# Performance work log

Measured on AMD Instinct MI355X. Metric: run time of the kernel, lower is better.

The kernel has to match this reference:

```python
import jax, jax.numpy as jnp
import numpy as np

N = 100000
E = 1600000
D = 128      # in_features
H = 128      # mlp hidden = out_features
O = 128      # out_features
BN_EPS = 1e-5

def _bn_train(x, gamma, beta):
    # BatchNorm1d in training mode: batch stats over node axis, biased variance
    mu = jnp.mean(x, axis=0)
    var = jnp.mean((x - mu) ** 2, axis=0)
    return (x - mu) * jax.lax.rsqrt(var + BN_EPS) * gamma + beta

def setup_inputs() -> dict:
    key = jax.random.key(0)
    ks = jax.random.split(key, 8)
    h = jax.random.normal(ks[0], (N, D), dtype=jnp.float32)
    edge_src = jax.random.randint(ks[1], (E,), 0, N, dtype=jnp.int32)
    edge_dst = jax.random.randint(ks[2], (E,), 0, N, dtype=jnp.int32)
    s1 = 1.0 / np.sqrt(D)
    s2 = 1.0 / np.sqrt(H)
    W1 = jax.random.uniform(ks[3], (D, H), jnp.float32, -s1, s1)
    b1 = jax.random.uniform(ks[4], (H,), jnp.float32, -s1, s1)
    W2 = jax.random.uniform(ks[5], (H, O), jnp.float32, -s2, s2)
    b2 = jax.random.uniform(ks[6], (O,), jnp.float32, -s2, s2)
    return {
        "h": h, "edge_src": edge_src, "edge_dst": edge_dst,
        "W1": W1, "b1": b1, "g1": jnp.ones((H,), jnp.float32), "be1": jnp.zeros((H,), jnp.float32),
        "W2": W2, "b2": b2, "g2": jnp.ones((O,), jnp.float32), "be2": jnp.zeros((O,), jnp.float32),
        "eps": jnp.zeros((), jnp.float32),
    }

def reference(h, edge_src, edge_dst, W1, b1, g1, be1, W2, b2, g2, be2, eps):
    # spmm(Adj, h) == scatter-add of gathered neighbor features
    msgs = h[edge_src]                                   # [E, D] irregular gather
    pooled = jax.ops.segment_sum(msgs, edge_dst, num_segments=N)  # [N, D]
    pooled = pooled + (1.0 + eps) * h                    # eps combine
    # MLP (2 layers): Linear -> BN -> ReLU -> Linear
    x = jax.nn.relu(_bn_train(pooled @ W1 + b1, g1, be1))
    x = x @ W2 + b2
    # final BN + ReLU
    return jax.nn.relu(_bn_train(x, g2, be2))
```

## Files before the change

kernel.cpp:

```cpp
#include <hip/hip_runtime.h>
#include <hip/hip_bf16.h>
#include <stdint.h>

#define BN_EPS 1e-5f
#define NSTRIPE 64

typedef __attribute__((ext_vector_type(8)))  short bf16x8;
typedef __attribute__((ext_vector_type(16))) float f32x16;

static __device__ __forceinline__ float bflo2f(uint32_t p){
  union { uint32_t u; float f; } c; c.u = p << 16; return c.f;
}
static __device__ __forceinline__ float bfhi2f(uint32_t p){
  union { uint32_t u; float f; } c; c.u = p & 0xffff0000u; return c.f;
}
static __device__ __forceinline__ uint16_t f2bf(float f){
  union { float f; uint32_t u; } c; c.f = f;
  uint32_t u = c.u;
  return (uint16_t)((u + 0x7fffu + ((u >> 16) & 1u)) >> 16);
}
static __device__ __forceinline__ uint32_t pack2(float a, float b){
  return (uint32_t)f2bf(a) | ((uint32_t)f2bf(b) << 16);
}

__global__ void k_prep(const float* __restrict__ h, uint16_t* __restrict__ hb, int hblocks,
                       const float* __restrict__ W1, const float* __restrict__ W2,
                       uint16_t* __restrict__ Wt1, uint16_t* __restrict__ Wt2,
                       float* __restrict__ stats,
                       const int* __restrict__ dst, int* __restrict__ M, int E, int NB){
  int b = blockIdx.x, t = threadIdx.x;
  if (b < hblocks){
    int i = (b * 256 + t) * 8;
    float4 a = *(const float4*)(h + i);
    float4 bb = *(const float4*)(h + i + 4);
    uint4 o;
    o.x = pack2(a.x, a.y); o.y = pack2(a.z, a.w);
    o.z = pack2(bb.x, bb.y); o.w = pack2(bb.z, bb.w);
    *(uint4*)(hb + i) = o;
    return;
  }
  if (b < hblocks + 16){
    int gid = (b - hblocks) * 256 + t;
    {
      float4 z = make_float4(0.f, 0.f, 0.f, 0.f);
      *(float4*)(stats + gid * 8) = z;
      *(float4*)(stats + gid * 8 + 4) = z;
    }
    const float* Wf = (gid < 2048) ? W1 : W2;
    uint16_t* Wt = (gid < 2048) ? Wt1 : Wt2;
    int cid = gid & 2047;
    int nrow = cid >> 4;
    int c    = cid & 15;
    int k0 = c * 8;
    float e[8];
    #pragma unroll
    for (int j = 0; j < 8; ++j) e[j] = Wf[(k0 + j) * 128 + nrow];
    uint4 o;
    o.x = pack2(e[0], e[1]); o.y = pack2(e[2], e[3]);
    o.z = pack2(e[4], e[5]); o.w = pack2(e[6], e[7]);
    int cs = c ^ (nrow & 15);
    *(uint4*)(Wt + nrow * 128 + cs * 8) = o;
    return;
  }
  int eb = b - hblocks - 16;
  __shared__ int cnt[512];
  cnt[t] = 0; cnt[t + 256] = 0;
  __syncthreads();
  int base = eb * 4096;
  #pragma unroll 4
  for (int j = t; j < 4096; j += 256){
    int i = base + j;
    if (i < E) atomicAdd(&cnt[dst[i] >> 8], 1);
  }
  __syncthreads();
  size_t row = (size_t)eb * NB;
  if (t < NB) M[row + t] = cnt[t];
  int t2 = t + 256;
  if (t2 < NB) M[row + t2] = cnt[t2];
}

__global__ void k_colscan(int* __restrict__ M, int* __restrict__ btot, int EB, int NB){
  __shared__ int s[256];
  int b = blockIdx.x, t = threadIdx.x;
  int i0 = 2 * t, i1 = 2 * t + 1;
  int v0 = (i0 < EB) ? M[(size_t)i0 * NB + b] : 0;
  int v1 = (i1 < EB) ? M[(size_t)i1 * NB + b] : 0;
  s[t] = v0 + v1;
  __syncthreads();
  for (int off = 1; off < 256; off <<= 1){
    int v = (t >= off) ? s[t - off] : 0;
    __syncthreads();
    s[t] += v;
    __syncthreads();
  }
  int excl = s[t] - (v0 + v1);
  if (i0 < EB) M[(size_t)i0 * NB + b] = excl;
  if (i1 < EB) M[(size_t)i1 * NB + b] = excl + v0;
  if (t == 255) btot[b] = s[255];
}

__global__ void k_bscan(const int* __restrict__ btot, int* __restrict__ bbase,
                        int* __restrict__ row_off, int NB, int n, int E){
  __shared__ int s[256];
  int t = threadIdx.x;
  int i0 = 2 * t, i1 = 2 * t + 1;
  int v0 = (i0 < NB) ? btot[i0] : 0;
  int v1 = (i1 < NB) ? btot[i1] : 0;
  s[t] = v0 + v1;
  __syncthreads();
  for (int off = 1; off < 256; off <<= 1){
    int v = (t >= off) ? s[t - off] : 0;
    __syncthreads();
    s[t] += v;
    __syncthreads();
  }
  int excl = s[t] - (v0 + v1);
  if (i0 < NB) bbase[i0] = excl;
  if (i1 < NB) bbase[i1] = excl + v0;
  if (t == 0){ bbase[NB] = E; row_off[n] = E; }
}

__global__ void k_bin(const int* __restrict__ src, const int* __restrict__ dst,
                      const int* __restrict__ M, const int* __restrict__ bbase,
                      uint2* __restrict__ binned, int E, int NB){
  __shared__ int comb[512];
  __shared__ int cur[512];
  int t = threadIdx.x;
  size_t row = (size_t)blockIdx.x * NB;
  if (t < NB) comb[t] = bbase[t] + M[row + t];
  int t2 = t + 256;
  if (t2 < NB) comb[t2] = bbase[t2] + M[row + t2];
  cur[t] = 0; cur[t + 256] = 0;
  __syncthreads();
  int base = blockIdx.x * 4096;
  #pragma unroll 4
  for (int j = t; j < 4096; j += 256){
    int i = base + j;
    if (i < E){
      int d = dst[i];
      int b = d >> 8;
      int r = atomicAdd(&cur[b], 1);
      binned[comb[b] + r] = make_uint2((unsigned)src[i], (unsigned)d);
    }
  }
}

__global__ void k_csr(const uint2* __restrict__ binned, const int* __restrict__ bbase,
                      int* __restrict__ row_off, int* __restrict__ col_idx, int n){
  __shared__ int cnt[256];
  __shared__ int off[256];
  __shared__ int cur[256];
  int b = blockIdx.x, t = threadIdx.x;
  int e0 = bbase[b], e1 = bbase[b + 1];
  int nb0 = b << 8;
  cnt[t] = 0; cur[t] = 0;
  __syncthreads();
  int m = e1 - e0;
  for (int j = t; j < m; j += 256) atomicAdd(&cnt[binned[e0 + j].y & 255], 1);
  __syncthreads();
  int v = cnt[t];
  off[t] = v;
  __syncthreads();
  for (int o = 1; o < 256; o <<= 1){
    int u = (t >= o) ? off[t - o] : 0;
    __syncthreads();
    off[t] += u;
    __syncthreads();
  }
  int excl = off[t] - v;
  __syncthreads();
  off[t] = excl;
  if (nb0 + t < n) row_off[nb0 + t] = e0 + excl;
  __syncthreads();
  for (int j = t; j < m; j += 256){
    uint2 p = binned[e0 + j];
    int dl = p.y & 255;
    int r = atomicAdd(&cur[dl], 1);
    col_idx[e0 + off[dl] + r] = (int)p.x;
  }
}

__global__ void k_gather(const uint16_t* __restrict__ hb, const int* __restrict__ row_off,
                         const int* __restrict__ col_idx, const float* __restrict__ eps_p,
                         uint16_t* __restrict__ Xb, int n){
  int node = (blockIdx.x << 2) + (threadIdx.x >> 6);
  int lane = threadIdx.x & 63;
  if (node >= n) return;
  int g = lane >> 4;
  int c = lane & 15;
  const uint4* hp4 = (const uint4*)hb;
  int j = row_off[node], jend = row_off[node + 1];
  float a0=0.f,a1=0.f,a2=0.f,a3=0.f,a4=0.f,a5=0.f,a6=0.f,a7=0.f;
  for (; j + 16 <= jend; j += 16){
    int sA = col_idx[j + g];
    int sB = col_idx[j + 4 + g];
    int sC = col_idx[j + 8 + g];
    int sD = col_idx[j + 12 + g];
    uint4 vA = hp4[(size_t)sA * 16 + c];
    uint4 vB = hp4[(size_t)sB * 16 + c];
    uint4 vC = hp4[(size_t)sC * 16 + c];
    uint4 vD = hp4[(size_t)sD * 16 + c];
    a0 += (bflo2f(vA.x) + bflo2f(vB.x)) + (bflo2f(vC.x) + bflo2f(vD.x));
    a1 += (bfhi2f(vA.x) + bfhi2f(vB.x)) + (bfhi2f(vC.x) + bfhi2f(vD.x));
    a2 += (bflo2f(vA.y) + bflo2f(vB.y)) + (bflo2f(vC.y) + bflo2f(vD.y));
    a3 += (bfhi2f(vA.y) + bfhi2f(vB.y)) + (bfhi2f(vC.y) + bfhi2f(vD.y));
    a4 += (bflo2f(vA.z) + bflo2f(vB.z)) + (bflo2f(vC.z) + bflo2f(vD.z));
    a5 += (bfhi2f(vA.z) + bfhi2f(vB.z)) + (bfhi2f(vC.z) + bfhi2f(vD.z));
    a6 += (bflo2f(vA.w) + bflo2f(vB.w)) + (bflo2f(vC.w) + bflo2f(vD.w));
    a7 += (bfhi2f(vA.w) + bfhi2f(vB.w)) + (bfhi2f(vC.w) + bfhi2f(vD.w));
  }
  for (; j + 8 <= jend; j += 8){
    int sA = col_idx[j + g];
    int sB = col_idx[j + 4 + g];
    uint4 vA = hp4[(size_t)sA * 16 + c];
    uint4 vB = hp4[(size_t)sB * 16 + c];
    a0 += bflo2f(vA.x) + bflo2f(vB.x);
    a1 += bfhi2f(vA.x) + bfhi2f(vB.x);
    a2 += bflo2f(vA.y) + bflo2f(vB.y);
    a3 += bfhi2f(vA.y) + bfhi2f(vB.y);
    a4 += bflo2f(vA.z) + bflo2f(vB.z);
    a5 += bfhi2f(vA.z) + bfhi2f(vB.z);
    a6 += bflo2f(vA.w) + bflo2f(vB.w);
    a7 += bfhi2f(vA.w) + bfhi2f(vB.w);
  }
  for (; j + 4 <= jend; j += 4){
    int s = col_idx[j + g];
    uint4 v = hp4[(size_t)s * 16 + c];
    a0 += bflo2f(v.x); a1 += bfhi2f(v.x);
    a2 += bflo2f(v.y); a3 += bfhi2f(v.y);
    a4 += bflo2f(v.z); a5 += bfhi2f(v.z);
    a6 += bflo2f(v.w); a7 += bfhi2f(v.w);
  }
  int rem = jend - j;
  if (rem > 0){
    int jj = j + (g < rem ? g : rem - 1);
    float w = (g < rem) ? 1.f : 0.f;
    int s = col_idx[jj];
    uint4 v = hp4[(size_t)s * 16 + c];
    a0 = fmaf(w, bflo2f(v.x), a0); a1 = fmaf(w, bfhi2f(v.x), a1);
    a2 = fmaf(w, bflo2f(v.y), a2); a3 = fmaf(w, bfhi2f(v.y), a3);
    a4 = fmaf(w, bflo2f(v.z), a4); a5 = fmaf(w, bfhi2f(v.z), a5);
    a6 = fmaf(w, bflo2f(v.w), a6); a7 = fmaf(w, bfhi2f(v.w), a7);
  }
  a0 += __shfl_xor(a0, 16); a1 += __shfl_xor(a1, 16);
  a2 += __shfl_xor(a2, 16); a3 += __shfl_xor(a3, 16);
  a4 += __shfl_xor(a4, 16); a5 += __shfl_xor(a5, 16);
  a6 += __shfl_xor(a6, 16); a7 += __shfl_xor(a7, 16);
  a0 += __shfl_xor(a0, 32); a1 += __shfl_xor(a1, 32);
  a2 += __shfl_xor(a2, 32); a3 += __shfl_xor(a3, 32);
  a4 += __shfl_xor(a4, 32); a5 += __shfl_xor(a5, 32);
  a6 += __shfl_xor(a6, 32); a7 += __shfl_xor(a7, 32);
  if (g == 0){
    float ce = 1.0f + eps_p[0];
    uint4 vh = hp4[(size_t)node * 16 + c];
    a0 = fmaf(ce, bflo2f(vh.x), a0); a1 = fmaf(ce, bfhi2f(vh.x), a1);
    a2 = fmaf(ce, bflo2f(vh.y), a2); a3 = fmaf(ce, bfhi2f(vh.y), a3);
    a4 = fmaf(ce, bflo2f(vh.z), a4); a5 = fmaf(ce, bfhi2f(vh.z), a5);
    a6 = fmaf(ce, bflo2f(vh.w), a6); a7 = fmaf(ce, bfhi2f(vh.w), a7);
    uint4 o;
    o.x = pack2(a0, a1); o.y = pack2(a2, a3);
    o.z = pack2(a4, a5); o.w = pack2(a6, a7);
    *((uint4*)Xb + (size_t)node * 16 + c) = o;
  }
}

template<bool BN_IN>
__global__ __launch_bounds__(256, 3) void k_mgemm(
    const uint16_t* __restrict__ Ag, const uint16_t* __restrict__ Wt,
    const float* __restrict__ bias_f,
    const float* __restrict__ sin_s, const float* __restrict__ sqin_s,
    const float* __restrict__ gin, const float* __restrict__ bein, float invN,
    uint16_t* __restrict__ Yout, float* __restrict__ osum_s, float* __restrict__ osq_s, int n){
  __shared__ __align__(16) uint16_t Al[64 * 128];
  __shared__ __align__(16) uint16_t Wl[128 * 128];
  __shared__ float csum[128], csq[128];
  __shared__ __align__(16) float ABl[256];
  int tid = threadIdx.x;
  int rbase = blockIdx.x * 64;
  int stripe = blockIdx.x & (NSTRIPE - 1);

  if (BN_IN){
    if (tid < 128){
      float s = 0.f, q = 0.f;
      #pragma unroll 8
      for (int st = 0; st < NSTRIPE; ++st){
        s += sin_s[st * 128 + tid];
        q += sqin_s[st * 128 + tid];
      }
      float mu = s * invN;
      float var = q * invN - mu * mu;
      float A = gin[tid] * rsqrtf(var + BN_EPS);
      ABl[tid] = A;
      ABl[128 + tid] = bein[tid] - mu * A;
    }
    __syncthreads();
  }

  {
    const uint4* g = (const uint4*)Wt;
    uint4* d = (uint4*)Wl;
    #pragma unroll
    for (int i = 0; i < 8; ++i) d[tid + 256 * i] = g[tid + 256 * i];
  }
  #pragma unroll
  for (int i = 0; i < 4; ++i){
    int f = tid + 256 * i;
    int m = f >> 4, c = f & 15;
    int gr = rbase + m;
    uint4 v = make_uint4(0, 0, 0, 0);
    if (gr < n){
      v = *(const uint4*)(Ag + (size_t)gr * 128 + c * 8);
      if (BN_IN){
        int k0 = c * 8;
        float4 ka0 = *(const float4*)(ABl + k0);
        float4 ka1 = *(const float4*)(ABl + k0 + 4);
        float4 kb0 = *(const float4*)(ABl + 128 + k0);
        float4 kb1 = *(const float4*)(ABl + 128 + k0 + 4);
        float e0 = fmaxf(fmaf(bflo2f(v.x), ka0.x, kb0.x), 0.f);
        float e1 = fmaxf(fmaf(bfhi2f(v.x), ka0.y, kb0.y), 0.f);
        float e2 = fmaxf(fmaf(bflo2f(v.y), ka0.z, kb0.z), 0.f);
        float e3 = fmaxf(fmaf(bfhi2f(v.y), ka0.w, kb0.w), 0.f);
        float e4 = fmaxf(fmaf(bflo2f(v.z), ka1.x, kb1.x), 0.f);
        float e5 = fmaxf(fmaf(bfhi2f(v.z), ka1.y, kb1.y), 0.f);
        float e6 = fmaxf(fmaf(bflo2f(v.w), ka1.z, kb1.z), 0.f);
        float e7 = fmaxf(fmaf(bfhi2f(v.w), ka1.w, kb1.w), 0.f);
        v.x = pack2(e0, e1); v.y = pack2(e2, e3);
        v.z = pack2(e4, e5); v.w = pack2(e6, e7);
      }
    }
    *(uint4*)((char*)Al + m * 256 + ((c ^ (m & 15)) * 16)) = v;
  }
  if (tid < 128){ csum[tid] = 0.f; csq[tid] = 0.f; }
  __syncthreads();

  int lane = tid & 63;
  int w    = tid >> 6;
  int hi   = lane >> 5;
  int key  = lane & 15;
  int m0   = (w & 1) * 32;
  int n0   = (w >> 1) * 64;
  int mrow = m0 + (lane & 31);
  int nrow0 = n0 + (lane & 31);
  int nrow1 = nrow0 + 32;

  f32x16 acc0, acc1;
  #pragma unroll
  for (int i = 0; i < 16; ++i){ acc0[i] = 0.f; acc1[i] = 0.f; }

  const char* Ab = (const char*)Al;
  const char* Wb = (const char*)Wl;
  #pragma unroll
  for (int kt = 0; kt < 8; ++kt){
    int cs = ((2 * kt + hi) ^ key) * 16;
    bf16x8 a  = *(const bf16x8*)(Ab + mrow  * 256 + cs);
    bf16x8 b0 = *(const bf16x8*)(Wb + nrow0 * 256 + cs);
    bf16x8 b1 = *(const bf16x8*)(Wb + nrow1 * 256 + cs);
    acc0 = __builtin_amdgcn_mfma_f32_32x32x16_bf16(a, b0, acc0, 0, 0, 0);
    acc1 = __builtin_amdgcn_mfma_f32_32x32x16_bf16(a, b1, acc1, 0, 0, 0);
  }
  __syncthreads();

  uint16_t* Yl = Wl;
  float bias0 = bias_f[nrow0];
  float bias1 = bias_f[nrow1];
  float ps0 = 0.f, pq0 = 0.f, ps1 = 0.f, pq1 = 0.f;
  #pragma unroll
  for (int r = 0; r < 16; ++r){
    int row = m0 + (r & 3) + 8 * (r >> 2) + 4 * hi;
    bool valid = (rbase + row) < n;
    float y0 = acc0[r] + bias0;
    float y1 = acc1[r] + bias1;
    if (valid){
      ps0 += y0; pq0 += y0 * y0;
      ps1 += y1; pq1 += y1 * y1;
    }
    Yl[row * 128 + nrow0] = f2bf(y0);
    Yl[row * 128 + nrow1] = f2bf(y1);
  }
  atomicAdd(&csum[nrow0], ps0); atomicAdd(&csq[nrow0], pq0);
  atomicAdd(&csum[nrow1], ps1); atomicAdd(&csq[nrow1], pq1);
  __syncthreads();

  #pragma unroll
  for (int i = 0; i < 4; ++i){
    int id = tid + 256 * i;
    int row = id >> 4, c = id & 15;
    int gr = rbase + row;
    if (gr < n)
      *((uint4*)Yout + (size_t)gr * 16 + c) = *((const uint4*)Yl + id);
  }
  if (tid < 128){
    atomicAdd(&osum_s[stripe * 128 + tid], csum[tid]);
    atomicAdd(&osq_s[stripe * 128 + tid], csq[tid]);
  }
}

__global__ void k_bncoef2(const float* __restrict__ sum_s, const float* __restrict__ sq_s,
                          const float* __restrict__ g, const float* __restrict__ be,
                          float* __restrict__ AB, float invN){
  int c = threadIdx.x;
  if (c < 128){
    float s = 0.f, q = 0.f;
    #pragma unroll 8
    for (int st = 0; st < NSTRIPE; ++st){
      s += sum_s[st * 128 + c];
      q += sq_s[st * 128 + c];
    }
    float mu = s * invN;
    float var = q * invN - mu * mu;
    float A = g[c] * rsqrtf(var + BN_EPS);
    AB[c] = A;
    AB[128 + c] = be[c] - mu * A;
  }
}

__global__ void k_final(const uint16_t* __restrict__ Y2b, const float* __restrict__ ABg,
                        float* __restrict__ out, int total){
  __shared__ __align__(16) float AB[256];
  int tid = threadIdx.x;
  if (tid < 64){
    *(float4*)(AB + tid * 4) = *(const float4*)(ABg + tid * 4);
  }
  __syncthreads();
  int i = (blockIdx.x * 256 + tid) * 4;
  if (i >= total) return;
  uint2 v = *(const uint2*)(Y2b + i);
  int c = i & 127;
  float4 a = *(const float4*)(AB + c);
  float4 b = *(const float4*)(AB + 128 + c);
  float4 o;
  o.x = fmaxf(fmaf(bflo2f(v.x), a.x, b.x), 0.f);
  o.y = fmaxf(fmaf(bfhi2f(v.x), a.y, b.y), 0.f);
  o.z = fmaxf(fmaf(bflo2f(v.y), a.z, b.z), 0.f);
  o.w = fmaxf(fmaf(bfhi2f(v.y), a.w, b.w), 0.f);
  *(float4*)(out + i) = o;
}

extern "C" void kernel_launch(void* const* d_in, const int* in_sizes, int n_in,
                              void* d_out, int out_size, void* d_ws, size_t ws_size,
                              hipStream_t stream){
  const float* h    = (const float*)d_in[0];
  const int*   esrc = (const int*)d_in[1];
  const int*   edst = (const int*)d_in[2];
  const float* W1   = (const float*)d_in[3];
  const float* b1   = (const float*)d_in[4];
  const float* g1   = (const float*)d_in[5];
  const float* be1  = (const float*)d_in[6];
  const float* W2   = (const float*)d_in[7];
  const float* b2   = (const float*)d_in[8];
  const float* g2   = (const float*)d_in[9];
  const float* be2  = (const float*)d_in[10];
  const float* eps  = (const float*)d_in[11];
  int n = in_sizes[0] / 128;
  int E = in_sizes[1];
  (void)n_in; (void)out_size; (void)ws_size;

  int NB = (n + 255) >> 8;
  int EB = (E + 4095) >> 12;

  char* ws = (char*)d_ws;
  size_t off = 0;
  auto alloc = [&](size_t bytes) -> void* {
    void* p = ws + off;
    off += (bytes + 511) & ~(size_t)511;
    return p;
  };
  size_t feat_b = (size_t)n * 128 * 2;
  uint16_t* B1   = (uint16_t*)alloc(feat_b);
  uint16_t* B2   = (uint16_t*)alloc(feat_b);
  int*   row_off = (int*)alloc((size_t)(n + 1) * 4);
  int*   col_idx = (int*)alloc((size_t)E * 4);
  int*   M       = (int*)alloc((size_t)EB * NB * 4);
  int*   btot    = (int*)alloc((size_t)(NB + 1) * 4);
  int*   bbase   = (int*)alloc((size_t)(NB + 1) * 4);
  float* stats   = (float*)alloc((size_t)4 * NSTRIPE * 128 * 4);
  float* AB2     = (float*)alloc(256 * 4);
  uint16_t* Wt1  = (uint16_t*)alloc(128 * 128 * 2);
  uint16_t* Wt2  = (uint16_t*)alloc(128 * 128 * 2);
  float* sum1 = stats;
  float* sq1  = stats + NSTRIPE * 128;
  float* sum2 = stats + 2 * NSTRIPE * 128;
  float* sq2  = stats + 3 * NSTRIPE * 128;
  uint16_t* hb  = B1;
  uint2*   binned = (uint2*)B2;
  uint16_t* Xb  = B2;
  uint16_t* Y1b = B1;
  uint16_t* Y2b = B2;

  int total = n * 128;
  int hblocks = total / 8 / 256;
  float invN = 1.0f / (float)n;

  k_prep<<<hblocks + 16 + EB, 256, 0, stream>>>(h, hb, hblocks, W1, W2, Wt1, Wt2,
                                                stats, edst, M, E, NB);
  k_colscan<<<NB, 256, 0, stream>>>(M, btot, EB, NB);
  k_bscan  <<<1, 256, 0, stream>>>(btot, bbase, row_off, NB, n, E);
  k_bin    <<<EB, 256, 0, stream>>>(esrc, edst, M, bbase, binned, E, NB);
  k_csr    <<<NB, 256, 0, stream>>>(binned, bbase, row_off, col_idx, n);

  k_gather<<<(n + 3) / 4, 256, 0, stream>>>(hb, row_off, col_idx, eps, Xb, n);

  int gblocks = (n + 63) / 64;
  k_mgemm<false><<<gblocks, 256, 0, stream>>>(Xb, Wt1, b1,
      nullptr, nullptr, nullptr, nullptr, 0.f, Y1b, sum1, sq1, n);
  k_mgemm<true> <<<gblocks, 256, 0, stream>>>(Y1b, Wt2, b2,
      sum1, sq1, g1, be1, invN, Y2b, sum2, sq2, n);

  k_bncoef2<<<1, 128, 0, stream>>>(sum2, sq2, g2, be2, AB2, invN);
  k_final<<<(total / 4 + 255) / 256, 256, 0, stream>>>(Y2b, AB2, (float*)d_out, total);
}
```

Baseline: 309.9 us.

## Fuse neighbor gather into first GEMM and read weights from global

Merges the gather/aggregation kernel with the first MFMA GEMM: each block aggregates 64 node rows directly into shared memory and multiplies by W1. This removes the intermediate pooled-feature write and read and one kernel launch. Both GEMM kernels also stop staging the transposed weights in LDS and read B fragments straight from global (unswizzled layout), which cuts LDS use to allow higher occupancy. The trade-off is less parallelism in the gather phase (each wave handles 16 nodes serially) and B operands now come through L1/L2 instead of LDS.

```diff
diff --git a/kernel.cpp b/kernel.cpp
--- a/kernel.cpp
+++ b/kernel.cpp
@@ -58,8 +58,7 @@
     uint4 o;
     o.x = pack2(e[0], e[1]); o.y = pack2(e[2], e[3]);
     o.z = pack2(e[4], e[5]); o.w = pack2(e[6], e[7]);
-    int cs = c ^ (nrow & 15);
-    *(uint4*)(Wt + nrow * 128 + cs * 8) = o;
+    *(uint4*)(Wt + nrow * 128 + c * 8) = o;
     return;
   }
   int eb = b - hblocks - 16;
@@ -180,128 +179,180 @@
   }
 }
 
-__global__ void k_gather(const uint16_t* __restrict__ hb, const int* __restrict__ row_off,
-                         const int* __restrict__ col_idx, const float* __restrict__ eps_p,
-                         uint16_t* __restrict__ Xb, int n){
-  int node = (blockIdx.x << 2) + (threadIdx.x >> 6);
-  int lane = threadIdx.x & 63;
-  if (node >= n) return;
+__global__ __launch_bounds__(256, 4) void k_gg(
+    const uint16_t* __restrict__ hb, const int* __restrict__ row_off,
+    const int* __restrict__ col_idx, const float* __restrict__ eps_p,
+    const uint16_t* __restrict__ Wt, const float* __restrict__ bias_f,
+    uint16_t* __restrict__ Yout, float* __restrict__ osum_s, float* __restrict__ osq_s, int n){
+  __shared__ __align__(16) uint16_t Al[64 * 128];
+  __shared__ float csum[128], csq[128];
+  int tid = threadIdx.x;
+  int rbase = blockIdx.x * 64;
+  int stripe = blockIdx.x & (NSTRIPE - 1);
+  int lane = tid & 63;
+  int w    = tid >> 6;
   int g = lane >> 4;
   int c = lane & 15;
   const uint4* hp4 = (const uint4*)hb;
-  int j = row_off[node], jend = row_off[node + 1];
-  float a0=0.f,a1=0.f,a2=0.f,a3=0.f,a4=0.f,a5=0.f,a6=0.f,a7=0.f;
-  for (; j + 16 <= jend; j += 16){
-    int sA = col_idx[j + g];
-    int sB = col_idx[j + 4 + g];
-    int sC = col_idx[j + 8 + g];
-    int sD = col_idx[j + 12 + g];
-    uint4 vA = hp4[(size_t)sA * 16 + c];
-    uint4 vB = hp4[(size_t)sB * 16 + c];
-    uint4 vC = hp4[(size_t)sC * 16 + c];
-    uint4 vD = hp4[(size_t)sD * 16 + c];
-    a0 += (bflo2f(vA.x) + bflo2f(vB.x)) + (bflo2f(vC.x) + bflo2f(vD.x));
-    a1 += (bfhi2f(vA.x) + bfhi2f(vB.x)) + (bfhi2f(vC.x) + bfhi2f(vD.x));
-    a2 += (bflo2f(vA.y) + bflo2f(vB.y)) + (bflo2f(vC.y) + bflo2f(vD.y));
-    a3 += (bfhi2f(vA.y) + bfhi2f(vB.y)) + (bfhi2f(vC.y) + bfhi2f(vD.y));
-    a4 += (bflo2f(vA.z) + bflo2f(vB.z)) + (bflo2f(vC.z) + bflo2f(vD.z));
-    a5 += (bfhi2f(vA.z) + bfhi2f(vB.z)) + (bfhi2f(vC.z) + bfhi2f(vD.z));
-    a6 += (bflo2f(vA.w) + bflo2f(vB.w)) + (bflo2f(vC.w) + bflo2f(vD.w));
-    a7 += (bfhi2f(vA.w) + bfhi2f(vB.w)) + (bfhi2f(vC.w) + bfhi2f(vD.w));
-  }
-  for (; j + 8 <= jend; j += 8){
-    int sA = col_idx[j + g];
-    int sB = col_idx[j + 4 + g];
-    uint4 vA = hp4[(size_t)sA * 16 + c];
-    uint4 vB = hp4[(size_t)sB * 16 + c];
-    a0 += bflo2f(vA.x) + bflo2f(vB.x);
-    a1 += bfhi2f(vA.x) + bfhi2f(vB.x);
-    a2 += bflo2f(vA.y) + bflo2f(vB.y);
-    a3 += bfhi2f(vA.y) + bfhi2f(vB.y);
-    a4 += bflo2f(vA.z) + bflo2f(vB.z);
-    a5 += bfhi2f(vA.z) + bfhi2f(vB.z);
-    a6 += bflo2f(vA.w) + bflo2f(vB.w);
-    a7 += bfhi2f(vA.w) + bfhi2f(vB.w);
-  }
-  for (; j + 4 <= jend; j += 4){
-    int s = col_idx[j + g];
-    uint4 v = hp4[(size_t)s * 16 + c];
-    a0 += bflo2f(v.x); a1 += bfhi2f(v.x);
-    a2 += bflo2f(v.y); a3 += bfhi2f(v.y);
-    a4 += bflo2f(v.z); a5 += bfhi2f(v.z);
-    a6 += bflo2f(v.w); a7 += bfhi2f(v.w);
-  }
-  int rem = jend - j;
-  if (rem > 0){
-    int jj = j + (g < rem ? g : rem - 1);
-    float w = (g < rem) ? 1.f : 0.f;
-    int s = col_idx[jj];
-    uint4 v = hp4[(size_t)s * 16 + c];
-    a0 = fmaf(w, bflo2f(v.x), a0); a1 = fmaf(w, bfhi2f(v.x), a1);
-    a2 = fmaf(w, bflo2f(v.y), a2); a3 = fmaf(w, bfhi2f(v.y), a3);
-    a4 = fmaf(w, bflo2f(v.z), a4); a5 = fmaf(w, bfhi2f(v.z), a5);
-    a6 = fmaf(w, bflo2f(v.w), a6); a7 = fmaf(w, bfhi2f(v.w), a7);
-  }
-  a0 += __shfl_xor(a0, 16); a1 += __shfl_xor(a1, 16);
-  a2 += __shfl_xor(a2, 16); a3 += __shfl_xor(a3, 16);
-  a4 += __shfl_xor(a4, 16); a5 += __shfl_xor(a5, 16);
-  a6 += __shfl_xor(a6, 16); a7 += __shfl_xor(a7, 16);
-  a0 += __shfl_xor(a0, 32); a1 += __shfl_xor(a1, 32);
-  a2 += __shfl_xor(a2, 32); a3 += __shfl_xor(a3, 32);
-  a4 += __shfl_xor(a4, 32); a5 += __shfl_xor(a5, 32);
-  a6 += __shfl_xor(a6, 32); a7 += __shfl_xor(a7, 32);
-  if (g == 0){
-    float ce = 1.0f + eps_p[0];
-    uint4 vh = hp4[(size_t)node * 16 + c];
-    a0 = fmaf(ce, bflo2f(vh.x), a0); a1 = fmaf(ce, bfhi2f(vh.x), a1);
-    a2 = fmaf(ce, bflo2f(vh.y), a2); a3 = fmaf(ce, bfhi2f(vh.y), a3);
-    a4 = fmaf(ce, bflo2f(vh.z), a4); a5 = fmaf(ce, bfhi2f(vh.z), a5);
-    a6 = fmaf(ce, bflo2f(vh.w), a6); a7 = fmaf(ce, bfhi2f(vh.w), a7);
-    uint4 o;
-    o.x = pack2(a0, a1); o.y = pack2(a2, a3);
-    o.z = pack2(a4, a5); o.w = pack2(a6, a7);
-    *((uint4*)Xb + (size_t)node * 16 + c) = o;
-  }
-}
-
-template<bool BN_IN>
-__global__ __launch_bounds__(256, 3) void k_mgemm(
+  float ce = 1.0f + eps_p[0];
+  if (tid < 128){ csum[tid] = 0.f; csq[tid] = 0.f; }
+
+  for (int it = 0; it < 16; ++it){
+    int m = w * 16 + it;
+    int gr = rbase + m;
+    float a0=0.f,a1=0.f,a2=0.f,a3=0.f,a4=0.f,a5=0.f,a6=0.f,a7=0.f;
+    if (gr < n){
+      int j = row_off[gr], jend = row_off[gr + 1];
+      for (; j + 16 <= jend; j += 16){
+        int sA = col_idx[j + g];
+        int sB = col_idx[j + 4 + g];
+        int sC = col_idx[j + 8 + g];
+        int sD = col_idx[j + 12 + g];
+        uint4 vA = hp4[(size_t)sA * 16 + c];
+        uint4 vB = hp4[(size_t)sB * 16 + c];
+        uint4 vC = hp4[(size_t)sC * 16 + c];
+        uint4 vD = hp4[(size_t)sD * 16 + c];
+        a0 += (bflo2f(vA.x) + bflo2f(vB.x)) + (bflo2f(vC.x) + bflo2f(vD.x));
+        a1 += (bfhi2f(vA.x) + bfhi2f(vB.x)) + (bfhi2f(vC.x) + bfhi2f(vD.x));
+        a2 += (bflo2f(vA.y) + bflo2f(vB.y)) + (bflo2f(vC.y) + bflo2f(vD.y));
+        a3 += (bfhi2f(vA.y) + bfhi2f(vB.y)) + (bfhi2f(vC.y) + bfhi2f(vD.y));
+        a4 += (bflo2f(vA.z) + bflo2f(vB.z)) + (bflo2f(vC.z) + bflo2f(vD.z));
+        a5 += (bfhi2f(vA.z) + bfhi2f(vB.z)) + (bfhi2f(vC.z) + bfhi2f(vD.z));
+        a6 += (bflo2f(vA.w) + bflo2f(vB.w)) + (bflo2f(vC.w) + bflo2f(vD.w));
+        a7 += (bfhi2f(vA.w) + bfhi2f(vB.w)) + (bfhi2f(vC.w) + bfhi2f(vD.w));
+      }
+      for (; j + 4 <= jend; j += 4){
+        int s = col_idx[j + g];
+        uint4 v = hp4[(size_t)s * 16 + c];
+        a0 += bflo2f(v.x); a1 += bfhi2f(v.x);
+        a2 += bflo2f(v.y); a3 += bfhi2f(v.y);
+        a4 += bflo2f(v.z); a5 += bfhi2f(v.z);
+        a6 += bflo2f(v.w); a7 += bfhi2f(v.w);
+      }
+      int rem = jend - j;
+      if (rem > 0){
+        int jj = j + (g < rem ? g : rem - 1);
+        float wq = (g < rem) ? 1.f : 0.f;
+        int s = col_idx[jj];
+        uint4 v = hp4[(size_t)s * 16 + c];
+        a0 = fmaf(wq, bflo2f(v.x), a0); a1 = fmaf(wq, bfhi2f(v.x), a1);
+        a2 = fmaf(wq, bflo2f(v.y), a2); a3 = fmaf(wq, bfhi2f(v.y), a3);
+        a4 = fmaf(wq, bflo2f(v.z), a4); a5 = fmaf(wq, bfhi2f(v.z), a5);
+        a6 = fmaf(wq, bflo2f(v.w), a6); a7 = fmaf(wq, bfhi2f(v.w), a7);
+      }
+      a0 += __shfl_xor(a0, 16); a1 += __shfl_xor(a1, 16);
+      a2 += __shfl_xor(a2, 16); a3 += __shfl_xor(a3, 16);
+      a4 += __shfl_xor(a4, 16); a5 += __shfl_xor(a5, 16);
+      a6 += __shfl_xor(a6, 16); a7 += __shfl_xor(a7, 16);
+      a0 += __shfl_xor(a0, 32); a1 += __shfl_xor(a1, 32);
+      a2 += __shfl_xor(a2, 32); a3 += __shfl_xor(a3, 32);
+      a4 += __shfl_xor(a4, 32); a5 += __shfl_xor(a5, 32);
+      a6 += __shfl_xor(a6, 32); a7 += __shfl_xor(a7, 32);
+      if (g == 0){
+        uint4 vh = hp4[(size_t)gr * 16 + c];
+        a0 = fmaf(ce, bflo2f(vh.x), a0); a1 = fmaf(ce, bfhi2f(vh.x), a1);
+        a2 = fmaf(ce, bflo2f(vh.y), a2); a3 = fmaf(ce, bfhi2f(vh.y), a3);
+        a4 = fmaf(ce, bflo2f(vh.z), a4); a5 = fmaf(ce, bfhi2f(vh.z), a5);
+        a6 = fmaf(ce, bflo2f(vh.w), a6); a7 = fmaf(ce, bfhi2f(vh.w), a7);
+      }
+    }
+    if (g == 0){
+      uint4 o;
+      o.x = pack2(a0, a1); o.y = pack2(a2, a3);
+      o.z = pack2(a4, a5); o.w = pack2(a6, a7);
+      *(uint4*)((char*)Al + m * 256 + ((c ^ (m & 15)) * 16)) = o;
+    }
+  }
+  __syncthreads();
+
+  int hi   = lane >> 5;
+  int key  = lane & 15;
+  int m0   = (w & 1) * 32;
+  int n0   = (w >> 1) * 64;
+  int mrow = m0 + (lane & 31);
+  int nrow0 = n0 + (lane & 31);
+  int nrow1 = nrow0 + 32;
+
+  f32x16 acc0, acc1;
+  #pragma unroll
+  for (int i = 0; i < 16; ++i){ acc0[i] = 0.f; acc1[i] = 0.f; }
+
+  const char* Ab = (const char*)Al;
+  #pragma unroll
+  for (int kt = 0; kt < 8; ++kt){
+    int ck = 2 * kt + hi;
+    bf16x8 a  = *(const bf16x8*)(Ab + mrow * 256 + ((ck ^ key) * 16));
+    bf16x8 b0 = *(const bf16x8*)(Wt + nrow0 * 128 + ck * 8);
+    bf16x8 b1 = *(const bf16x8*)(Wt + nrow1 * 128 + ck * 8);
+    acc0 = __builtin_amdgcn_mfma_f32_32x32x16_bf16(a, b0, acc0, 0, 0, 0);
+    acc1 = __builtin_amdgcn_mfma_f32_32x32x16_bf16(a, b1, acc1, 0, 0, 0);
+  }
+  __syncthreads();
+
+  uint16_t* Yl = Al;
+  float bias0 = bias_f[nrow0];
+  float bias1 = bias_f[nrow1];
+  float ps0 = 0.f, pq0 = 0.f, ps1 = 0.f, pq1 = 0.f;
+  #pragma unroll
+  for (int r = 0; r < 16; ++r){
+    int row = m0 + (r & 3) + 8 * (r >> 2) + 4 * hi;
+    bool valid = (rbase + row) < n;
+    float y0 = acc0[r] + bias0;
+    float y1 = acc1[r] + bias1;
+    if (valid){
+      ps0 += y0; pq0 += y0 * y0;
+      ps1 += y1; pq1 += y1 * y1;
+    }
+    Yl[row * 128 + nrow0] = f2bf(y0);
+    Yl[row * 128 + nrow1] = f2bf(y1);
+  }
+  atomicAdd(&csum[nrow0], ps0); atomicAdd(&csq[nrow0], pq0);
+  atomicAdd(&csum[nrow1], ps1); atomicAdd(&csq[nrow1], pq1);
+  __syncthreads();
+
+  #pragma unroll
+  for (int i = 0; i < 4; ++i){
+    int id = tid + 256 * i;
+    int row = id >> 4, cc = id & 15;
+    int gr = rbase + row;
+    if (gr < n)
+      *((uint4*)Yout + (size_t)gr * 16 + cc) = *((const uint4*)Yl + id);
+  }
+  if (tid < 128){
+    atomicAdd(&osum_s[stripe * 128 + tid], csum[tid]);
+    atomicAdd(&osq_s[stripe * 128 + tid], csq[tid]);
+  }
+}
+
+__global__ __launch_bounds__(256, 4) void k_mgemm2(
     const uint16_t* __restrict__ Ag, const uint16_t* __restrict__ Wt,
     const float* __restrict__ bias_f,
     const float* __restrict__ sin_s, const float* __restrict__ sqin_s,
     const float* __restrict__ gin, const float* __restrict__ bein, float invN,
     uint16_t* __restrict__ Yout, float* __restrict__ osum_s, float* __restrict__ osq_s, int n){
   __shared__ __align__(16) uint16_t Al[64 * 128];
-  __shared__ __align__(16) uint16_t Wl[128 * 128];
   __shared__ float csum[128], csq[128];
   __shared__ __align__(16) float ABl[256];
   int tid = threadIdx.x;
   int rbase = blockIdx.x * 64;
   int stripe = blockIdx.x & (NSTRIPE - 1);
 
-  if (BN_IN){
-    if (tid < 128){
-      float s = 0.f, q = 0.f;
-      #pragma unroll 8
-      for (int st = 0; st < NSTRIPE; ++st){
-        s += sin_s[st * 128 + tid];
-        q += sqin_s[st * 128 + tid];
-      }
-      float mu = s * invN;
-      float var = q * invN - mu * mu;
-      float A = gin[tid] * rsqrtf(var + BN_EPS);
-      ABl[tid] = A;
-      ABl[128 + tid] = bein[tid] - mu * A;
-    }
-    __syncthreads();
-  }
-
-  {
-    const uint4* g = (const uint4*)Wt;
-    uint4* d = (uint4*)Wl;
-    #pragma unroll
-    for (int i = 0; i < 8; ++i) d[tid + 256 * i] = g[tid + 256 * i];
-  }
+  if (tid < 128){
+    float s = 0.f, q = 0.f;
+    #pragma unroll 8
+    for (int st = 0; st < NSTRIPE; ++st){
+      s += sin_s[st * 128 + tid];
+      q += sqin_s[st * 128 + tid];
+    }
+    float mu = s * invN;
+    float var = q * invN - mu * mu;
+    float A = gin[tid] * rsqrtf(var + BN_EPS);
+    ABl[tid] = A;
+    ABl[128 + tid] = bein[tid] - mu * A;
+    csum[tid] = 0.f; csq[tid] = 0.f;
+  }
+  __syncthreads();
+
   #pragma unroll
   for (int i = 0; i < 4; ++i){
     int f = tid + 256 * i;
@@ -310,27 +361,24 @@
     uint4 v = make_uint4(0, 0, 0, 0);
     if (gr < n){
       v = *(const uint4*)(Ag + (size_t)gr * 128 + c * 8);
-      if (BN_IN){
-        int k0 = c * 8;
-        float4 ka0 = *(const float4*)(ABl + k0);
-        float4 ka1 = *(const float4*)(ABl + k0 + 4);
-        float4 kb0 = *(const float4*)(ABl + 128 + k0);
-        float4 kb1 = *(const float4*)(ABl + 128 + k0 + 4);
-        float e0 = fmaxf(fmaf(bflo2f(v.x), ka0.x, kb0.x), 0.f);
-        float e1 = fmaxf(fmaf(bfhi2f(v.x), ka0.y, kb0.y), 0.f);
-        float e2 = fmaxf(fmaf(bflo2f(v.y), ka0.z, kb0.z), 0.f);
-        float e3 = fmaxf(fmaf(bfhi2f(v.y), ka0.w, kb0.w), 0.f);
-        float e4 = fmaxf(fmaf(bflo2f(v.z), ka1.x, kb1.x), 0.f);
-        float e5 = fmaxf(fmaf(bfhi2f(v.z), ka1.y, kb1.y), 0.f);
-        float e6 = fmaxf(fmaf(bflo2f(v.w), ka1.z, kb1.z), 0.f);
-        float e7 = fmaxf(fmaf(bfhi2f(v.w), ka1.w, kb1.w), 0.f);
-        v.x = pack2(e0, e1); v.y = pack2(e2, e3);
-        v.z = pack2(e4, e5); v.w = pack2(e6, e7);
-      }
+      int k0 = c * 8;
+      float4 ka0 = *(const float4*)(ABl + k0);
+      float4 ka1 = *(const float4*)(ABl + k0 + 4);
+      float4 kb0 = *(const float4*)(ABl + 128 + k0);
+      float4 kb1 = *(const float4*)(ABl + 128 + k0 + 4);
+      float e0 = fmaxf(fmaf(bflo2f(v.x), ka0.x, kb0.x), 0.f);
+      float e1 = fmaxf(fmaf(bfhi2f(v.x), ka0.y, kb0.y), 0.f);
+      float e2 = fmaxf(fmaf(bflo2f(v.y), ka0.z, kb0.z), 0.f);
+      float e3 = fmaxf(fmaf(bfhi2f(v.y), ka0.w, kb0.w), 0.f);
+      float e4 = fmaxf(fmaf(bflo2f(v.z), ka1.x, kb1.x), 0.f);
+      float e5 = fmaxf(fmaf(bfhi2f(v.z), ka1.y, kb1.y), 0.f);
+      float e6 = fmaxf(fmaf(bflo2f(v.w), ka1.z, kb1.z), 0.f);
+      float e7 = fmaxf(fmaf(bfhi2f(v.w), ka1.w, kb1.w), 0.f);
+      v.x = pack2(e0, e1); v.y = pack2(e2, e3);
+      v.z = pack2(e4, e5); v.w = pack2(e6, e7);
     }
     *(uint4*)((char*)Al + m * 256 + ((c ^ (m & 15)) * 16)) = v;
   }
-  if (tid < 128){ csum[tid] = 0.f; csq[tid] = 0.f; }
   __syncthreads();
 
   int lane = tid & 63;
@@ -348,19 +396,18 @@
   for (int i = 0; i < 16; ++i){ acc0[i] = 0.f; acc1[i] = 0.f; }
 
   const char* Ab = (const char*)Al;
-  const char* Wb = (const char*)Wl;
   #pragma unroll
   for (int kt = 0; kt < 8; ++kt){
-    int cs = ((2 * kt + hi) ^ key) * 16;
-    bf16x8 a  = *(const bf16x8*)(Ab + mrow  * 256 + cs);
-    bf16x8 b0 = *(const bf16x8*)(Wb + nrow0 * 256 + cs);
-    bf16x8 b1 = *(const bf16x8*)(Wb + nrow1 * 256 + cs);
+    int ck = 2 * kt + hi;
+    bf16x8 a  = *(const bf16x8*)(Ab + mrow * 256 + ((ck ^ key) * 16));
+    bf16x8 b0 = *(const bf16x8*)(Wt + nrow0 * 128 + ck * 8);
+    bf16x8 b1 = *(const bf16x8*)(Wt + nrow1 * 128 + ck * 8);
     acc0 = __builtin_amdgcn_mfma_f32_32x32x16_bf16(a, b0, acc0, 0, 0, 0);
     acc1 = __builtin_amdgcn_mfma_f32_32x32x16_bf16(a, b1, acc1, 0, 0, 0);
   }
   __syncthreads();
 
-  uint16_t* Yl = Wl;
+  uint16_t* Yl = Al;
   float bias0 = bias_f[nrow0];
   float bias1 = bias_f[nrow1];
   float ps0 = 0.f, pq0 = 0.f, ps1 = 0.f, pq1 = 0.f;
@@ -384,10 +431,10 @@
   #pragma unroll
   for (int i = 0; i < 4; ++i){
     int id = tid + 256 * i;
-    int row = id >> 4, c = id & 15;
+    int row = id >> 4, cc = id & 15;
     int gr = rbase + row;
     if (gr < n)
-      *((uint4*)Yout + (size_t)gr * 16 + c) = *((const uint4*)Yl + id);
+      *((uint4*)Yout + (size_t)gr * 16 + cc) = *((const uint4*)Yl + id);
   }
   if (tid < 128){
     atomicAdd(&osum_s[stripe * 128 + tid], csum[tid]);
@@ -483,9 +530,8 @@
   float* sq2  = stats + 3 * NSTRIPE * 128;
   uint16_t* hb  = B1;
   uint2*   binned = (uint2*)B2;
-  uint16_t* Xb  = B2;
-  uint16_t* Y1b = B1;
-  uint16_t* Y2b = B2;
+  uint16_t* Y1b = B2;
+  uint16_t* Y2b = B1;
 
   int total = n * 128;
   int hblocks = total / 8 / 256;
@@ -498,12 +544,10 @@
   k_bin    <<<EB, 256, 0, stream>>>(esrc, edst, M, bbase, binned, E, NB);
   k_csr    <<<NB, 256, 0, stream>>>(binned, bbase, row_off, col_idx, n);
 
-  k_gather<<<(n + 3) / 4, 256, 0, stream>>>(hb, row_off, col_idx, eps, Xb, n);
-
   int gblocks = (n + 63) / 64;
-  k_mgemm<false><<<gblocks, 256, 0, stream>>>(Xb, Wt1, b1,
-      nullptr, nullptr, nullptr, nullptr, 0.f, Y1b, sum1, sq1, n);
-  k_mgemm<true> <<<gblocks, 256, 0, stream>>>(Y1b, Wt2, b2,
+  k_gg<<<gblocks, 256, 0, stream>>>(hb, row_off, col_idx, eps, Wt1, b1,
+                                    Y1b, sum1, sq1, n);
+  k_mgemm2<<<gblocks, 256, 0, stream>>>(Y1b, Wt2, b2,
       sum1, sq1, g1, be1, invN, Y2b, sum2, sq2, n);
 
   k_bncoef2<<<1, 128, 0, stream>>>(sum2, sq2, g2, be2, AB2, invN);
```

Measured after the change: 305.3 us. About the same (-1.5%).
